# Optimization experiments

Hardware: AMD Instinct MI355X
Metric: run time of the kernel (lower is better)

The kernel has to match this reference:

```python
import jax, jax.numpy as jnp
import numpy as np

D_MODEL = 1024
N_HEADS = 16
D_HEAD = D_MODEL // N_HEADS
WINDOW = 256
SCALE = D_HEAD ** -0.5


def setup_inputs() -> dict:
    key = jax.random.key(0)
    ks = jax.random.split(key, 5)
    B, S = 2, 2048
    x = jax.random.normal(ks[0], (B, S, D_MODEL), dtype=jnp.float32)
    # weights stored as [d_in, d_out] so forward is x @ W + b
    W_qkv = jax.random.normal(ks[1], (D_MODEL, 3 * D_MODEL), dtype=jnp.float32) * (D_MODEL ** -0.5)
    b_qkv = jnp.zeros((3 * D_MODEL,), dtype=jnp.float32)
    W_out = jax.random.normal(ks[2], (D_MODEL, D_MODEL), dtype=jnp.float32) * (D_MODEL ** -0.5)
    b_out = jnp.zeros((D_MODEL,), dtype=jnp.float32)
    return {"x": x, "W_qkv": W_qkv, "b_qkv": b_qkv, "W_out": W_out, "b_out": b_out}


def _window_mask(S):
    # Faithful to source: keep positions where (i <= j) & (i >= j - WINDOW + 1),
    # i = query index (rows), j = key index (cols). (Anti-causal window, as in repo.)
    idx = jnp.arange(S)
    keep = (idx[:, None] <= idx[None, :]) & (idx[:, None] >= idx[None, :] - WINDOW + 1)
    return keep  # [S, S] bool


def reference(x, W_qkv, b_qkv, W_out, b_out):
    B, S, D = x.shape
    qkv = x @ W_qkv + b_qkv                      # [B,S,3D]
    q, k, v = jnp.split(qkv, 3, axis=-1)
    def heads(t):
        return t.reshape(B, S, N_HEADS, D_HEAD).transpose(0, 2, 1, 3)  # [B,H,S,dh]
    q, k, v = heads(q), heads(k), heads(v)
    attn = jnp.einsum('bhid,bhjd->bhij', q, k) * SCALE  # [B,H,S,S]
    keep = _window_mask(S)
    attn = jnp.where(keep[None, None], attn, -jnp.inf)
    attn = jax.nn.softmax(attn, axis=-1)
    # dropout is identity in eval mode
    out = jnp.einsum('bhij,bhjd->bhid', attn, v)        # [B,H,S,dh]
    out = out.transpose(0, 2, 1, 3).reshape(B, S, D)
    return out @ W_out + b_out
```

## Files before the change

kernel.cpp:

```cpp
#include <hip/hip_runtime.h>

typedef __bf16 bf16x8 __attribute__((ext_vector_type(8)));
typedef float f32x4 __attribute__((ext_vector_type(4)));
typedef unsigned short u16x8 __attribute__((ext_vector_type(8)));
typedef unsigned short u16x4 __attribute__((ext_vector_type(4)));

#define MFMA16(a, b, c) __builtin_amdgcn_mfma_f32_16x16x32_bf16((a), (b), (c), 0, 0, 0)

__device__ __forceinline__ unsigned short f2bf(float f) {
  union { float f; unsigned int i; } v; v.f = f;
  unsigned int u = v.i;
  u += 0x7fffu + ((u >> 16) & 1u);
  return (unsigned short)(u >> 16);
}

__device__ __forceinline__ void gload16(const void* g, void* l) {
  __builtin_amdgcn_global_load_lds(
      (const __attribute__((address_space(1))) unsigned int*)g,
      (__attribute__((address_space(3))) unsigned int*)l, 16, 0, 0);
}

__global__ __launch_bounds__(256) void convert_x(const float* __restrict__ X,
                                                 unsigned short* __restrict__ Xb) {
  size_t i = (size_t)(blockIdx.x * 256 + threadIdx.x) * 8;
  f32x4 f0 = *(const f32x4*)(X + i);
  f32x4 f1 = *(const f32x4*)(X + i + 4);
  u16x8 t;
#pragma unroll
  for (int j = 0; j < 4; ++j) { t[j] = f2bf(f0[j]); t[4 + j] = f2bf(f1[j]); }
  *(u16x8*)(Xb + i) = t;
}

__global__ __launch_bounds__(256) void transpose_w(const float* __restrict__ W,
                                                   unsigned short* __restrict__ Wt,
                                                   int N) {
  __shared__ unsigned short t[32][33];
  int tx = threadIdx.x & 31, ty = threadIdx.x >> 5;
  int bx = blockIdx.x;
  int by = blockIdx.y;
#pragma unroll
  for (int j = 0; j < 4; ++j) {
    int r = ty + j * 8;
    t[tx][r] = f2bf(W[(size_t)(by * 32 + r) * N + bx * 32 + tx]);
  }
  __syncthreads();
#pragma unroll
  for (int j = 0; j < 4; ++j) {
    int r = ty + j * 8;
    Wt[(size_t)(bx * 32 + r) * 1024 + by * 32 + tx] = t[r][tx];
  }
}

__global__ __launch_bounds__(512) void gemm_bt(
    const unsigned short* __restrict__ A, const unsigned short* __restrict__ Bt,
    const float* __restrict__ bias,
    unsigned short* __restrict__ O0, unsigned short* __restrict__ O1,
    unsigned short* __restrict__ O2, float* __restrict__ OF, int mode) {
  __shared__ __align__(16) unsigned short As0[128 * 32];
  __shared__ __align__(16) unsigned short Bs0[128 * 32];
  __shared__ __align__(16) unsigned short As1[128 * 32];
  __shared__ __align__(16) unsigned short Bs1[128 * 32];

  const int K = 1024;
  int tid = threadIdx.x;
  int lane = tid & 63, wave = tid >> 6, quad = lane >> 4, l16 = lane & 15;
  int wr = wave >> 2, wc = wave & 3;
  int m0 = blockIdx.x * 128, n0 = blockIdx.y * 128;

  int srow = tid >> 2, su = tid & 3;
  const unsigned short* ag = A + (size_t)(m0 + srow) * K + su * 8;
  const unsigned short* bg = Bt + (size_t)(n0 + srow) * K + su * 8;
  int loff = tid * 16;

  int abase = (wr * 64 + l16) * 64 + quad * 16;
  int bbase = (wc * 32 + l16) * 64 + quad * 16;

  f32x4 acc[4][2];
#pragma unroll
  for (int i = 0; i < 4; ++i)
#pragma unroll
    for (int j = 0; j < 2; ++j) acc[i][j] = f32x4{0.f, 0.f, 0.f, 0.f};

  auto STAGE = [&](int k0, char* Asb, char* Bsb) {
    gload16(ag + k0, Asb + loff);
    gload16(bg + k0, Bsb + loff);
  };
  auto COMPUTE = [&](const char* Asb, const char* Bsb) {
    bf16x8 af[4], bfr[2];
#pragma unroll
    for (int t = 0; t < 4; ++t)
      af[t] = *(const bf16x8*)(Asb + abase + t * 1024);
#pragma unroll
    for (int t = 0; t < 2; ++t)
      bfr[t] = *(const bf16x8*)(Bsb + bbase + t * 1024);
#pragma unroll
    for (int mt = 0; mt < 4; ++mt)
#pragma unroll
      for (int nt = 0; nt < 2; ++nt)
        acc[mt][nt] = MFMA16(af[mt], bfr[nt], acc[mt][nt]);
  };
#define WAIT_VM2  asm volatile("s_waitcnt vmcnt(2)" ::: "memory")
#define WAIT_VM0  asm volatile("s_waitcnt vmcnt(0)" ::: "memory")
#define WAIT_LGKM asm volatile("s_waitcnt lgkmcnt(0)" ::: "memory")
#define BAR       __builtin_amdgcn_s_barrier()

  STAGE(0, (char*)As0, (char*)Bs0);
  for (int t = 0; t < 30; t += 2) {
    STAGE((t + 1) * 32, (char*)As1, (char*)Bs1);
    WAIT_VM2; BAR;
    COMPUTE((const char*)As0, (const char*)Bs0);
    WAIT_LGKM; BAR;
    STAGE((t + 2) * 32, (char*)As0, (char*)Bs0);
    WAIT_VM2; BAR;
    COMPUTE((const char*)As1, (const char*)Bs1);
    WAIT_LGKM; BAR;
  }
  STAGE(31 * 32, (char*)As1, (char*)Bs1);
  WAIT_VM2; BAR;
  COMPUTE((const char*)As0, (const char*)Bs0);
  WAIT_LGKM; BAR;
  WAIT_VM0; BAR;
  COMPUTE((const char*)As1, (const char*)Bs1);

  if (mode == 0) {
#pragma unroll
    for (int nt = 0; nt < 2; ++nt) {
      int n = n0 + wc * 32 + nt * 16 + l16;
      float bv = bias[n];
      int seg = n >> 10, cc = n & 1023, hh = cc >> 6, d = cc & 63;
#pragma unroll
      for (int mt = 0; mt < 4; ++mt) {
        int mb = m0 + wr * 64 + mt * 16 + quad * 4;
        int b = mb >> 11, s = mb & 2047;
        if (seg == 2) {
          u16x4 pk;
#pragma unroll
          for (int r = 0; r < 4; ++r) pk[r] = f2bf(acc[mt][nt][r] + bv);
          *(u16x4*)&O2[((size_t)((b << 4) + hh) * 64 + d) * 2048 + s] = pk;
        } else {
          unsigned short* O = seg ? O1 : O0;
#pragma unroll
          for (int r = 0; r < 4; ++r)
            O[((size_t)((b << 4) + hh) * 2048 + (s + r)) * 64 + d] = f2bf(acc[mt][nt][r] + bv);
        }
      }
    }
  } else {
#pragma unroll
    for (int nt = 0; nt < 2; ++nt) {
      int n = n0 + wc * 32 + nt * 16 + l16;
      float bv = bias[n];
#pragma unroll
      for (int mt = 0; mt < 4; ++mt) {
        int mb = m0 + wr * 64 + mt * 16 + quad * 4;
#pragma unroll
        for (int r = 0; r < 4; ++r)
          OF[(size_t)(mb + r) * 1024 + n] = acc[mt][nt][r] + bv;
      }
    }
  }
}

__global__ __launch_bounds__(256) void attn_kernel(
    const unsigned short* __restrict__ Q, const unsigned short* __restrict__ Kq,
    const unsigned short* __restrict__ Vt, unsigned short* __restrict__ AO) {
  __shared__ __align__(16) unsigned short Ps[4][16][40];

  int bid = blockIdx.x;
  int qblk = bid & 31, h = (bid >> 5) & 15, b = bid >> 9;
  int q0 = qblk * 64;
  int tid = threadIdx.x, lane = tid & 63, wave = tid >> 6, quad = lane >> 4, l16 = lane & 15;

  const unsigned short* Qb = Q + (size_t)(((b << 4) + h) * 2048) * 64;
  const unsigned short* Kb = Kq + (size_t)(((b << 4) + h) * 2048) * 64;
  const unsigned short* Vb = Vt + (size_t)(((b << 4) + h) * 64) * 2048;

  int qrow = q0 + wave * 16 + l16;
  bf16x8 qf0 = __builtin_bit_cast(bf16x8, *(const u16x8*)&Qb[(size_t)qrow * 64 + quad * 8]);
  bf16x8 qf1 = __builtin_bit_cast(bf16x8, *(const u16x8*)&Qb[(size_t)qrow * 64 + 32 + quad * 8]);

  float mrow[4], lrow[4];
  f32x4 zero = {0.f, 0.f, 0.f, 0.f};
  f32x4 o[4];
#pragma unroll
  for (int i = 0; i < 4; ++i) o[i] = zero;
#pragma unroll
  for (int r = 0; r < 4; ++r) { mrow[r] = -1e30f; lrow[r] = 0.f; }

  const float SCALE = 0.125f;
  int pstart = (wave >= 2) ? 1 : 0;
  int pend = pstart + 8;

  for (int p = pstart; p <= pend; ++p) {
    int kbase = q0 + p * 32;

    f32x4 sc[2];
    __builtin_amdgcn_s_setprio(1);
#pragma unroll
    for (int t = 0; t < 2; ++t) {
      int krow = kbase + t * 16 + l16;
      krow = krow > 2047 ? 2047 : krow;
      bf16x8 kf0 = __builtin_bit_cast(bf16x8, *(const u16x8*)&Kb[(size_t)krow * 64 + quad * 8]);
      bf16x8 kf1 = __builtin_bit_cast(bf16x8, *(const u16x8*)&Kb[(size_t)krow * 64 + 32 + quad * 8]);
      f32x4 z = zero;
      z = MFMA16(qf0, kf0, z);
      z = MFMA16(qf1, kf1, z);
      sc[t] = z;
    }
    __builtin_amdgcn_s_setprio(0);

    float sv[2][4];
#pragma unroll
    for (int t = 0; t < 2; ++t)
#pragma unroll
      for (int r = 0; r < 4; ++r) {
        int kg = kbase + t * 16 + l16;
        int qg = q0 + wave * 16 + quad * 4 + r;
        bool valid = (kg >= qg) && (kg <= qg + 255) && (kg < 2048);
        sv[t][r] = valid ? sc[t][r] * SCALE : -1e30f;
      }
#pragma unroll
    for (int r = 0; r < 4; ++r) {
      float v = fmaxf(sv[0][r], sv[1][r]);
      v = fmaxf(v, __shfl_xor(v, 1));
      v = fmaxf(v, __shfl_xor(v, 2));
      v = fmaxf(v, __shfl_xor(v, 4));
      v = fmaxf(v, __shfl_xor(v, 8));
      float mnew = fmaxf(mrow[r], v);
      float alpha = __expf(mrow[r] - mnew);
      mrow[r] = mnew;
      float p0 = __expf(sv[0][r] - mnew);
      float p1 = __expf(sv[1][r] - mnew);
      p0 = (sv[0][r] > -5e29f) ? p0 : 0.f;
      p1 = (sv[1][r] > -5e29f) ? p1 : 0.f;
      float rs = p0 + p1;
      rs += __shfl_xor(rs, 1);
      rs += __shfl_xor(rs, 2);
      rs += __shfl_xor(rs, 4);
      rs += __shfl_xor(rs, 8);
      lrow[r] = lrow[r] * alpha + rs;
#pragma unroll
      for (int nt = 0; nt < 4; ++nt) o[nt][r] *= alpha;
      Ps[wave][quad * 4 + r][l16] = f2bf(p0);
      Ps[wave][quad * 4 + r][16 + l16] = f2bf(p1);
    }
    __threadfence_block();
    bf16x8 pf = __builtin_bit_cast(bf16x8, *(const u16x8*)&Ps[wave][l16][quad * 8]);

    int vcol = kbase + quad * 8;
    vcol = vcol > 2040 ? 2040 : vcol;
    __builtin_amdgcn_s_setprio(1);
#pragma unroll
    for (int nt = 0; nt < 4; ++nt) {
      int vrow = nt * 16 + l16;
      bf16x8 vf = __builtin_bit_cast(bf16x8, *(const u16x8*)&Vb[(size_t)vrow * 2048 + vcol]);
      o[nt] = MFMA16(pf, vf, o[nt]);
    }
    __builtin_amdgcn_s_setprio(0);
  }

  unsigned short* dst = AO + ((size_t)(b * 2048 + q0 + wave * 16) * 1024) + h * 64;
#pragma unroll
  for (int nt = 0; nt < 4; ++nt)
#pragma unroll
    for (int r = 0; r < 4; ++r) {
      int qq = quad * 4 + r;
      dst[(size_t)qq * 1024 + nt * 16 + l16] = f2bf(o[nt][r] / lrow[r]);
    }
}

extern "C" void kernel_launch(void* const* d_in, const int* in_sizes, int n_in,
                              void* d_out, int out_size, void* d_ws, size_t ws_size,
                              hipStream_t stream) {
  const float* x = (const float*)d_in[0];
  const float* W_qkv = (const float*)d_in[1];
  const float* b_qkv = (const float*)d_in[2];
  const float* W_out = (const float*)d_in[3];
  const float* b_out = (const float*)d_in[4];
  float* out = (float*)d_out;

  unsigned short* ws = (unsigned short*)d_ws;
  unsigned short* Qw  = ws;
  unsigned short* Kw  = ws + 4194304;
  unsigned short* Vw  = ws + 8388608;
  unsigned short* Wqt = ws + 12582912;
  unsigned short* AO  = ws + 12582912;
  unsigned short* Wot = ws;
  unsigned short* Xb  = (unsigned short*)d_out;

  dim3 blk(256);
  dim3 gblk(512);
  convert_x<<<dim3(2048), blk, 0, stream>>>(x, Xb);
  transpose_w<<<dim3(96, 32), blk, 0, stream>>>(W_qkv, Wqt, 3072);
  gemm_bt<<<dim3(32, 24), gblk, 0, stream>>>(Xb, Wqt, b_qkv, Qw, Kw, Vw, nullptr, 0);
  attn_kernel<<<dim3(1024), blk, 0, stream>>>(Qw, Kw, Vw, AO);
  transpose_w<<<dim3(32, 32), blk, 0, stream>>>(W_out, Wot, 1024);
  gemm_bt<<<dim3(32, 8), gblk, 0, stream>>>(AO, Wot, b_out, nullptr, nullptr, nullptr, out, 1);
}
```

Baseline: 174.1 us.

## Widen attention key step to 64 and double-buffer K register prefetch

The attention inner loop now handles 64 keys per iteration: 5 fully unrolled steps instead of 9 steps of 32 with a per-wave start offset. K fragments for the next step are loaded into a second register buffer while the current step runs softmax. All V fragments for the step are loaded at the top of the iteration, before the QK MFMAs. The aim is to hide global-load latency behind compute and to halve the per-step softmax and shuffle overhead. In exchange, register pressure rises, and waves 2-3 do a little masked extra work because all waves now share the same key range.

```diff
diff --git a/kernel.cpp b/kernel.cpp
--- a/kernel.cpp
+++ b/kernel.cpp
@@ -164,7 +164,7 @@
 __global__ __launch_bounds__(256) void attn_kernel(
     const unsigned short* __restrict__ Q, const unsigned short* __restrict__ Kq,
     const unsigned short* __restrict__ Vt, unsigned short* __restrict__ AO) {
-  __shared__ __align__(16) unsigned short Ps[4][16][40];
+  __shared__ __align__(16) unsigned short Ps[4][16][72];
 
   int bid = blockIdx.x;
   int qblk = bid & 31, h = (bid >> 5) & 15, b = bid >> 9;
@@ -188,40 +188,65 @@
   for (int r = 0; r < 4; ++r) { mrow[r] = -1e30f; lrow[r] = 0.f; }
 
   const float SCALE = 0.125f;
-  int pstart = (wave >= 2) ? 1 : 0;
-  int pend = pstart + 8;
-
-  for (int p = pstart; p <= pend; ++p) {
-    int kbase = q0 + p * 32;
-
-    f32x4 sc[2];
+  int qg0 = q0 + wave * 16 + quad * 4;
+
+  bf16x8 kf[2][4][2];
+#define LOADK(kb, kd)                                                          \
+  {                                                                            \
+    _Pragma("unroll") for (int t = 0; t < 4; ++t) {                            \
+      int krow = (kb) + t * 16 + l16;                                          \
+      krow = krow > 2047 ? 2047 : krow;                                        \
+      kd[t][0] = __builtin_bit_cast(bf16x8,                                    \
+          *(const u16x8*)&Kb[(size_t)krow * 64 + quad * 8]);                   \
+      kd[t][1] = __builtin_bit_cast(bf16x8,                                    \
+          *(const u16x8*)&Kb[(size_t)krow * 64 + 32 + quad * 8]);              \
+    }                                                                          \
+  }
+
+  LOADK(q0, kf[0]);
+
+#pragma unroll
+  for (int p = 0; p < 5; ++p) {
+    int kbase = q0 + p * 64;
+    int cur = p & 1, nxt = cur ^ 1;
+
+    bf16x8 vf[4][2];
+#pragma unroll
+    for (int nt = 0; nt < 4; ++nt)
+#pragma unroll
+      for (int s = 0; s < 2; ++s) {
+        int vcol = kbase + s * 32 + quad * 8;
+        vcol = vcol > 2040 ? 2040 : vcol;
+        vf[nt][s] = __builtin_bit_cast(bf16x8,
+            *(const u16x8*)&Vb[(size_t)(nt * 16 + l16) * 2048 + vcol]);
+      }
+
+    f32x4 sc[4];
     __builtin_amdgcn_s_setprio(1);
 #pragma unroll
-    for (int t = 0; t < 2; ++t) {
-      int krow = kbase + t * 16 + l16;
-      krow = krow > 2047 ? 2047 : krow;
-      bf16x8 kf0 = __builtin_bit_cast(bf16x8, *(const u16x8*)&Kb[(size_t)krow * 64 + quad * 8]);
-      bf16x8 kf1 = __builtin_bit_cast(bf16x8, *(const u16x8*)&Kb[(size_t)krow * 64 + 32 + quad * 8]);
+    for (int t = 0; t < 4; ++t) {
       f32x4 z = zero;
-      z = MFMA16(qf0, kf0, z);
-      z = MFMA16(qf1, kf1, z);
+      z = MFMA16(qf0, kf[cur][t][0], z);
+      z = MFMA16(qf1, kf[cur][t][1], z);
       sc[t] = z;
     }
     __builtin_amdgcn_s_setprio(0);
 
-    float sv[2][4];
-#pragma unroll
-    for (int t = 0; t < 2; ++t)
+    if (p < 4) LOADK(kbase + 64, kf[nxt]);
+
+    float sv[4][4];
+#pragma unroll
+    for (int t = 0; t < 4; ++t)
 #pragma unroll
       for (int r = 0; r < 4; ++r) {
         int kg = kbase + t * 16 + l16;
-        int qg = q0 + wave * 16 + quad * 4 + r;
+        int qg = qg0 + r;
         bool valid = (kg >= qg) && (kg <= qg + 255) && (kg < 2048);
         sv[t][r] = valid ? sc[t][r] * SCALE : -1e30f;
       }
 #pragma unroll
     for (int r = 0; r < 4; ++r) {
-      float v = fmaxf(sv[0][r], sv[1][r]);
+      float v = fmaxf(fmaxf(sv[0][r], sv[1][r]), fmaxf(sv[2][r], sv[3][r]));
       v = fmaxf(v, __shfl_xor(v, 1));
       v = fmaxf(v, __shfl_xor(v, 2));
       v = fmaxf(v, __shfl_xor(v, 4));
@@ -229,11 +254,13 @@
       float mnew = fmaxf(mrow[r], v);
       float alpha = __expf(mrow[r] - mnew);
       mrow[r] = mnew;
-      float p0 = __expf(sv[0][r] - mnew);
-      float p1 = __expf(sv[1][r] - mnew);
-      p0 = (sv[0][r] > -5e29f) ? p0 : 0.f;
-      p1 = (sv[1][r] > -5e29f) ? p1 : 0.f;
-      float rs = p0 + p1;
+      float pe[4];
+#pragma unroll
+      for (int t = 0; t < 4; ++t) {
+        float e = __expf(sv[t][r] - mnew);
+        pe[t] = (sv[t][r] > -5e29f) ? e : 0.f;
+      }
+      float rs = (pe[0] + pe[1]) + (pe[2] + pe[3]);
       rs += __shfl_xor(rs, 1);
       rs += __shfl_xor(rs, 2);
       rs += __shfl_xor(rs, 4);
@@ -241,20 +268,19 @@
       lrow[r] = lrow[r] * alpha + rs;
 #pragma unroll
       for (int nt = 0; nt < 4; ++nt) o[nt][r] *= alpha;
-      Ps[wave][quad * 4 + r][l16] = f2bf(p0);
-      Ps[wave][quad * 4 + r][16 + l16] = f2bf(p1);
+#pragma unroll
+      for (int t = 0; t < 4; ++t)
+        Ps[wave][quad * 4 + r][t * 16 + l16] = f2bf(pe[t]);
     }
     __threadfence_block();
-    bf16x8 pf = __builtin_bit_cast(bf16x8, *(const u16x8*)&Ps[wave][l16][quad * 8]);
-
-    int vcol = kbase + quad * 8;
-    vcol = vcol > 2040 ? 2040 : vcol;
+    bf16x8 pf0 = __builtin_bit_cast(bf16x8, *(const u16x8*)&Ps[wave][l16][quad * 8]);
+    bf16x8 pf1 = __builtin_bit_cast(bf16x8, *(const u16x8*)&Ps[wave][l16][32 + quad * 8]);
+
     __builtin_amdgcn_s_setprio(1);
 #pragma unroll
     for (int nt = 0; nt < 4; ++nt) {
-      int vrow = nt * 16 + l16;
-      bf16x8 vf = __builtin_bit_cast(bf16x8, *(const u16x8*)&Vb[(size_t)vrow * 2048 + vcol]);
-      o[nt] = MFMA16(pf, vf, o[nt]);
+      o[nt] = MFMA16(pf0, vf[nt][0], o[nt]);
+      o[nt] = MFMA16(pf1, vf[nt][1], o[nt]);
     }
     __builtin_amdgcn_s_setprio(0);
   }
```

New measurement: 178.2 us. 2.4% more time.
